# Kernel tuning notes

Measured on AMD Instinct MI355X. Metric: run time of the kernel, lower is better.

The kernel has to match this reference:

```python
import jax, jax.numpy as jnp
import numpy as np

DIM = 512
HEADS = 8
DIM_HEAD = 64
B, N = 4, 2048
EPS = 1e-5


def setup_inputs() -> dict:
    key = jax.random.key(0)
    ks = jax.random.split(key, 6)
    s = 0.02
    x = jax.random.normal(ks[0], (B, N, DIM), dtype=jnp.float32)
    Wq = jax.random.normal(ks[1], (DIM, HEADS * DIM_HEAD), dtype=jnp.float32) * s
    Wkv = jax.random.normal(ks[2], (DIM, 2 * HEADS * DIM_HEAD), dtype=jnp.float32) * s
    Wo = jax.random.normal(ks[3], (HEADS * DIM_HEAD, DIM), dtype=jnp.float32) * s
    bo = jnp.zeros((DIM,), dtype=jnp.float32)
    # gating layer: torch init is weight=0, bias=1; randomize weight slightly for a nontrivial path
    Wg = jax.random.normal(ks[4], (DIM, HEADS * DIM_HEAD), dtype=jnp.float32) * s
    bg = jnp.ones((HEADS * DIM_HEAD,), dtype=jnp.float32)
    gamma = jnp.ones((DIM,), dtype=jnp.float32)
    beta = jnp.zeros((DIM,), dtype=jnp.float32)
    return {"x": x, "Wq": Wq, "Wkv": Wkv, "Wo": Wo, "bo": bo,
            "Wg": Wg, "bg": bg, "gamma": gamma, "beta": beta}


def reference(x, Wq, Wkv, Wo, bo, Wg, bg, gamma, beta):
    h, d = HEADS, DIM_HEAD
    scale = d ** -0.5
    b, n, _ = x.shape

    q = x @ Wq                                   # [b, n, h*d]
    kv = x @ Wkv                                 # [b, n, 2*h*d]
    k, v = jnp.split(kv, 2, axis=-1)

    def split_heads(t):
        return t.reshape(b, n, h, d).transpose(0, 2, 1, 3)  # [b, h, n, d]

    q = split_heads(q) * scale
    k = split_heads(k)
    v = split_heads(v)

    dots = jnp.einsum('bhid,bhjd->bhij', q, k)   # [b, h, n, n]
    attn = jax.nn.softmax(dots, axis=-1)
    out = jnp.einsum('bhij,bhjd->bhid', attn, v)  # [b, h, n, d]
    out = out.transpose(0, 2, 1, 3).reshape(b, n, h * d)

    gates = x @ Wg + bg                           # [b, n, h*d]
    out = out * jax.nn.sigmoid(gates)
    out = out @ Wo + bo                           # [b, n, dim]
    out = x + out

    # LayerNorm over last dim, eps=1e-5 (torch default)
    mu = jnp.mean(out, axis=-1, keepdims=True)
    var = jnp.var(out, axis=-1, keepdims=True)
    out = (out - mu) * jax.lax.rsqrt(var + EPS) * gamma + beta
    return out
```

## Files before the change

kernel.cpp:

```cpp
#include <hip/hip_runtime.h>
#include <hip/hip_bf16.h>
#include <stdint.h>
#include <stddef.h>

#define SEQ   2048
#define NBATCH 4
#define NHEAD  8
#define DMODEL 512

typedef __attribute__((ext_vector_type(8))) short bf16x8;
typedef __attribute__((ext_vector_type(4))) float f32x4;
typedef __attribute__((ext_vector_type(16))) float f32x16;

#define MFMA16(a, b, c) __builtin_amdgcn_mfma_f32_16x16x32_bf16(a, b, c, 0, 0, 0)
#define MFMA32(a, b, c) __builtin_amdgcn_mfma_f32_32x32x16_bf16(a, b, c, 0, 0, 0)

#define QSCALE 0.18033688011112042f

__device__ __forceinline__ float bf2f(ushort u) {
  union { uint32_t i; float f; } v; v.i = ((uint32_t)u) << 16; return v.f;
}
__device__ __forceinline__ ushort f2bf(float f) {
  union { float f; uint32_t i; } v; v.f = f;
  uint32_t u = v.i;
  return (ushort)((u + 0x7fffu + ((u >> 16) & 1u)) >> 16);
}
__device__ __forceinline__ uint32_t cvtpk(float lo, float hi) {
  uint32_t d;
  asm("v_cvt_pk_bf16_f32 %0, %1, %2" : "=v"(d) : "v"(lo), "v"(hi));
  return d;
}

#if __has_builtin(__builtin_amdgcn_global_load_lds)
__device__ __forceinline__ void gload16(const void* g, void* l) {
  __builtin_amdgcn_global_load_lds(
      (const __attribute__((address_space(1))) void*)g,
      (__attribute__((address_space(3))) void*)l, 16, 0, 0);
}
#define GLOAD_DIRECT 1
#else
#define GLOAD_DIRECT 0
#endif

__global__ __launch_bounds__(256) void cvt_k(const float* __restrict__ in,
                                             ushort* __restrict__ out, int n8) {
  int i = blockIdx.x * 256 + threadIdx.x;
  if (i >= n8) return;
  const float4* p = (const float4*)(in + (size_t)i * 8);
  float4 a = p[0], b = p[1];
  union { int4 v; ushort u[8]; } o;
  o.u[0] = f2bf(a.x); o.u[1] = f2bf(a.y); o.u[2] = f2bf(a.z); o.u[3] = f2bf(a.w);
  o.u[4] = f2bf(b.x); o.u[5] = f2bf(b.y); o.u[6] = f2bf(b.z); o.u[7] = f2bf(b.w);
  *(int4*)(out + (size_t)i * 8) = o.v;
}

__global__ __launch_bounds__(256) void wtrans_k(const float* __restrict__ Wq,
                                                const float* __restrict__ Wkv,
                                                const float* __restrict__ Wg,
                                                const float* __restrict__ Wo,
                                                ushort* __restrict__ WT,
                                                ushort* __restrict__ WoT) {
  __shared__ ushort tile[32][33];
  int bx = blockIdx.x;
  const float* W;
  ushort* dst;
  int N, nt;
  if (bx < 16)       { W = Wq;  dst = WT;              N = 512;  nt = bx; }
  else if (bx < 48)  { W = Wkv; dst = WT + 512 * 512;  N = 1024; nt = bx - 16; }
  else if (bx < 64)  { W = Wg;  dst = WT + 1536 * 512; N = 512;  nt = bx - 48; }
  else               { W = Wo;  dst = WoT;             N = 512;  nt = bx - 64; }
  int t = threadIdx.x;
  int n0 = nt * 32, k0 = blockIdx.y * 32;
  int r = t >> 3, c = (t & 7) * 4;
#pragma unroll
  for (int j = 0; j < 4; j++)
    tile[r][c + j] = f2bf(W[(size_t)(k0 + r) * N + n0 + c + j]);
  __syncthreads();
#pragma unroll
  for (int j = 0; j < 4; j++)
    dst[(size_t)(n0 + r) * 512 + k0 + c + j] = tile[c + j][r];
}

__global__ __launch_bounds__(256, 2) void gemm128_k(const ushort* __restrict__ A,
                                                    const ushort* __restrict__ Bt,
                                                    ushort* __restrict__ qb,
                                                    ushort* __restrict__ kb,
                                                    ushort* __restrict__ vT,
                                                    ushort* __restrict__ gsb,
                                                    float* __restrict__ yout,
                                                    const float* __restrict__ bias,
                                                    const float* __restrict__ res,
                                                    int op) {
  __shared__ __align__(16) ushort Sh[4 * 128 * 64];
#define ASB(p) (Sh + (p) * (128 * 64))
#define BSB(p) (Sh + 2 * (128 * 64) + (p) * (128 * 64))
  int t = threadIdx.x;
  int nb = gridDim.x * gridDim.y;
  int bid = blockIdx.y * gridDim.x + blockIdx.x;
  int swz = (bid & 7) * (nb >> 3) + (bid >> 3);
  int row0 = (swz / gridDim.x) * 128, col0 = (swz % gridDim.x) * 128;

  int w = t >> 6, l = t & 63, l31 = l & 31, hi = l >> 5;
  int wm = w >> 1, wn = w & 1;
  f32x16 acc[2][2] = {};

  int srow = t >> 3;
  int ssl = (t & 7) ^ (srow & 7);
  const ushort* Ag = A + (size_t)(row0 + srow) * 512 + ssl * 8;
  const ushort* Bg = Bt + (size_t)(col0 + srow) * 512 + ssl * 8;
  int wslot = __builtin_amdgcn_readfirstlane((t >> 6) << 6);

#if GLOAD_DIRECT
#define STG(p, kt)                                                              \
  do {                                                                          \
    gload16(Ag + (size_t)(kt) * 64 + 0 * 32 * 512, ASB(p) + (wslot +   0) * 8); \
    gload16(Ag + (size_t)(kt) * 64 + 1 * 32 * 512, ASB(p) + (wslot + 256) * 8); \
    gload16(Ag + (size_t)(kt) * 64 + 2 * 32 * 512, ASB(p) + (wslot + 512) * 8); \
    gload16(Ag + (size_t)(kt) * 64 + 3 * 32 * 512, ASB(p) + (wslot + 768) * 8); \
    gload16(Bg + (size_t)(kt) * 64 + 0 * 32 * 512, BSB(p) + (wslot +   0) * 8); \
    gload16(Bg + (size_t)(kt) * 64 + 1 * 32 * 512, BSB(p) + (wslot + 256) * 8); \
    gload16(Bg + (size_t)(kt) * 64 + 2 * 32 * 512, BSB(p) + (wslot + 512) * 8); \
    gload16(Bg + (size_t)(kt) * 64 + 3 * 32 * 512, BSB(p) + (wslot + 768) * 8); \
  } while (0)
#else
#define STG(p, kt)                                                                  \
  do {                                                                              \
    *(int4*)(ASB(p) + (t +   0) * 8) = *(const int4*)(Ag + (size_t)(kt) * 64);      \
    *(int4*)(ASB(p) + (t + 256) * 8) =                                              \
        *(const int4*)(Ag + (size_t)(kt) * 64 + 1 * 32 * 512);                      \
    *(int4*)(ASB(p) + (t + 512) * 8) =                                              \
        *(const int4*)(Ag + (size_t)(kt) * 64 + 2 * 32 * 512);                      \
    *(int4*)(ASB(p) + (t + 768) * 8) =                                              \
        *(const int4*)(Ag + (size_t)(kt) * 64 + 3 * 32 * 512);                      \
    *(int4*)(BSB(p) + (t +   0) * 8) = *(const int4*)(Bg + (size_t)(kt) * 64);      \
    *(int4*)(BSB(p) + (t + 256) * 8) =                                              \
        *(const int4*)(Bg + (size_t)(kt) * 64 + 1 * 32 * 512);                      \
    *(int4*)(BSB(p) + (t + 512) * 8) =                                              \
        *(const int4*)(Bg + (size_t)(kt) * 64 + 2 * 32 * 512);                      \
    *(int4*)(BSB(p) + (t + 768) * 8) =                                              \
        *(const int4*)(Bg + (size_t)(kt) * 64 + 3 * 32 * 512);                      \
  } while (0)
#endif

#define FRAG(Mb, r, s) \
  (*(const bf16x8*)(Mb + ((r) * 64) + ((((s) ^ ((r) & 7))) << 3)))

  STG(0, 0);
  __syncthreads();

  for (int kt = 0; kt < 8; kt++) {
    int p = kt & 1;
    if (kt < 7) STG(p ^ 1, kt + 1);

    bf16x8 bfrag[2][4];
#pragma unroll
    for (int cb = 0; cb < 2; cb++)
#pragma unroll
      for (int kk = 0; kk < 4; kk++)
        bfrag[cb][kk] = FRAG(BSB(p), wn * 64 + cb * 32 + l31, kk * 2 + hi);

    __builtin_amdgcn_s_setprio(1);
#pragma unroll
    for (int rb = 0; rb < 2; rb++) {
      bf16x8 af[4];
#pragma unroll
      for (int kk = 0; kk < 4; kk++)
        af[kk] = FRAG(ASB(p), wm * 64 + rb * 32 + l31, kk * 2 + hi);
#pragma unroll
      for (int kk = 0; kk < 4; kk++) {
        acc[rb][0] = MFMA32(af[kk], bfrag[0][kk], acc[rb][0]);
        acc[rb][1] = MFMA32(af[kk], bfrag[1][kk], acc[rb][1]);
      }
    }
    __builtin_amdgcn_s_setprio(0);

    if (kt < 7) __syncthreads();
  }
#undef STG
#undef FRAG

  if (op == 10 && col0 >= 1024 && col0 < 1536) {
    __syncthreads();
    ushort* lt = Sh;
#pragma unroll
    for (int rb = 0; rb < 2; rb++)
#pragma unroll
      for (int cb = 0; cb < 2; cb++)
#pragma unroll
        for (int e = 0; e < 16; e++) {
          int rr = (e & 3) + 8 * (e >> 2) + 4 * hi;
          int rowL = wm * 64 + rb * 32 + rr;
          int colL = wn * 64 + cb * 32 + l31;
          lt[colL * 136 + rowL] = f2bf(acc[rb][cb][e]);
        }
    __syncthreads();
    int b_ = row0 >> 11;
    int nb0 = row0 & 2047;
#pragma unroll
    for (int r = 0; r < 8; r++) {
      int lin = r * 256 + t;
      int dcol = lin >> 4, n8 = lin & 15;
      int vcol = (col0 - 1024) + dcol;
      int hh = vcol >> 6, dd = vcol & 63;
      bf16x8 v = *(const bf16x8*)(lt + dcol * 136 + n8 * 8);
      *(bf16x8*)(vT + (((size_t)(b_ * 8 + hh) * 64) + dd) * 2048 + nb0 + n8 * 8) = v;
    }
  } else {
#pragma unroll
    for (int rb = 0; rb < 2; rb++) {
#pragma unroll
      for (int cb = 0; cb < 2; cb++) {
#pragma unroll
        for (int e = 0; e < 16; e++) {
          int rr = (e & 3) + 8 * (e >> 2) + 4 * hi;
          int row = row0 + wm * 64 + rb * 32 + rr;
          int col = col0 + wn * 64 + cb * 32 + l31;
          float v = acc[rb][cb][e];
          if (op == 3) {
            v += bias[col] + res[(size_t)row * 512 + col];
            yout[(size_t)row * 512 + col] = v;
          } else {
            if (col0 < 512) {
              qb[(size_t)row * 512 + col] = f2bf(v * QSCALE);
            } else if (col0 < 1024) {
              kb[(size_t)row * 512 + (col - 512)] = f2bf(v);
            } else {
              v += bias[col - 1536];
              v = 1.f / (1.f + __expf(-v));
              gsb[(size_t)row * 512 + (col - 1536)] = f2bf(v);
            }
          }
        }
      }
    }
  }
#undef ASB
#undef BSB
}

__global__ __launch_bounds__(512) void attn_k(const ushort* __restrict__ q,
                                              const ushort* __restrict__ kbuf,
                                              const ushort* __restrict__ vT,
                                              const ushort* __restrict__ gs,
                                              ushort* __restrict__ gated) {
  __shared__ __align__(16) ushort Kl[2][64][72];
  __shared__ __align__(16) ushort Vl[2][64][72];
  int t = threadIdx.x;
  int bid = blockIdx.x;
  int swz = (bid & 7) * 32 + (bid >> 3);
  int qt = swz & 7, bh = swz >> 3;
  int b = bh >> 3, h = bh & 7;
  int q0 = qt * 256;
  int w = t >> 6, l = t & 63;
  int l31 = l & 31, hi = l >> 5;
  size_t base_n = (size_t)b * SEQ;

  const ushort* qp = q + (base_n + q0 + w * 32 + l31) * 512 + h * 64 + hi * 8;
  bf16x8 qf[4];
#pragma unroll
  for (int kd = 0; kd < 4; kd++)
    qf[kd] = *(const bf16x8*)(qp + kd * 16);

  bf16x8 vones;
#pragma unroll
  for (int j = 0; j < 8; j++) vones[j] = (short)0x3F80;

  f32x16 acco0 = {}, acco1 = {}, acco2 = {};

  int srow = t >> 3, c8 = (t & 7) * 8;
  const ushort* kg = kbuf + (base_n + srow) * 512 + h * 64 + c8;
  const ushort* vg = vT + ((size_t)bh * 64 + srow) * 2048 + c8;

  int4 kA = *(const int4*)(kg);
  int4 vA = *(const int4*)(vg);
  *(int4*)((char*)Kl[0] + srow * 144 + c8 * 2) = kA;
  *(int4*)((char*)Vl[0] + srow * 144 + c8 * 2) = vA;
  kA = *(const int4*)(kg + (size_t)64 * 512);
  vA = *(const int4*)(vg + 64);
  __syncthreads();

  int p = 0;
  for (int jt = 0; jt < SEQ / 64; jt++) {
    f32x16 s0 = {}, s1 = {};
    __builtin_amdgcn_s_setprio(1);
#pragma unroll
    for (int kd = 0; kd < 4; kd++) {
      bf16x8 k0 = *(const bf16x8*)((const char*)Kl[p] + l31 * 144 + kd * 32 + hi * 16);
      bf16x8 k1 = *(const bf16x8*)((const char*)Kl[p] + (32 + l31) * 144 + kd * 32 + hi * 16);
      s0 = MFMA32(k0, qf[kd], s0);
      s1 = MFMA32(k1, qf[kd], s1);
    }
    __builtin_amdgcn_s_setprio(0);

    if (jt < SEQ / 64 - 1) {
      *(int4*)((char*)Kl[p ^ 1] + srow * 144 + c8 * 2) = kA;
      *(int4*)((char*)Vl[p ^ 1] + srow * 144 + c8 * 2) = vA;
    }

    uint32_t pk[16];
#pragma unroll
    for (int sg = 0; sg < 4; sg++) {
#pragma unroll
      for (int u = 0; u < 2; u++) {
        float a = __builtin_amdgcn_exp2f(s0[(sg << 2) | (u << 1)]);
        float c = __builtin_amdgcn_exp2f(s0[(sg << 2) | (u << 1) | 1]);
        pk[sg * 2 + u] = cvtpk(a, c);
      }
    }
#pragma unroll
    for (int sg = 0; sg < 4; sg++) {
#pragma unroll
      for (int u = 0; u < 2; u++) {
        float a = __builtin_amdgcn_exp2f(s1[(sg << 2) | (u << 1)]);
        float c = __builtin_amdgcn_exp2f(s1[(sg << 2) | (u << 1) | 1]);
        pk[8 + sg * 2 + u] = cvtpk(a, c);
      }
    }

    __builtin_amdgcn_s_setprio(1);
#pragma unroll
    for (int jk = 0; jk < 4; jk++) {
      uint32_t x0 = pk[(2 * jk) * 2 + 0], y0 = pk[(2 * jk + 1) * 2 + 0];
      uint32_t x1 = pk[(2 * jk) * 2 + 1], y1 = pk[(2 * jk + 1) * 2 + 1];
      asm("v_permlane32_swap_b32 %0, %1" : "+v"(x0), "+v"(y0));
      asm("v_permlane32_swap_b32 %0, %1" : "+v"(x1), "+v"(y1));
      union { bf16x8 v; uint32_t u[4]; } pa;
      pa.u[0] = x0; pa.u[1] = x1; pa.u[2] = y0; pa.u[3] = y1;
      bf16x8 v0 = *(const bf16x8*)((const char*)Vl[p] + l31 * 144 + jk * 32 + hi * 16);
      bf16x8 v1 = *(const bf16x8*)((const char*)Vl[p] + (32 + l31) * 144 + jk * 32 + hi * 16);
      acco0 = MFMA32(pa.v, v0, acco0);
      acco1 = MFMA32(pa.v, v1, acco1);
      acco2 = MFMA32(pa.v, vones, acco2);
    }
    __builtin_amdgcn_s_setprio(0);

    if (jt < SEQ / 64 - 1) {
      __syncthreads();
      if (jt < SEQ / 64 - 2) {
        kA = *(const int4*)(kg + (size_t)(jt + 2) * 64 * 512);
        vA = *(const int4*)(vg + (jt + 2) * 64);
      }
      p ^= 1;
    }
  }

#pragma unroll
  for (int e = 0; e < 16; e++) {
    int qr = (e & 3) + 8 * (e >> 2) + 4 * hi;
    size_t row = base_n + q0 + w * 32 + qr;
    int col = h * 64 + l31;
    float rcp = 1.f / acco2[e];
    float v0 = acco0[e] * rcp * bf2f(gs[row * 512 + col]);
    float v1 = acco1[e] * rcp * bf2f(gs[row * 512 + col + 32]);
    gated[row * 512 + col] = f2bf(v0);
    gated[row * 512 + col + 32] = f2bf(v1);
  }
}

__global__ __launch_bounds__(256) void ln_k(const float* __restrict__ y,
                                            const float* __restrict__ gamma,
                                            const float* __restrict__ beta,
                                            float* __restrict__ out) {
  int w = threadIdx.x >> 6, l = threadIdx.x & 63;
  size_t row = (size_t)blockIdx.x * 4 + w;
  const float4* yp = (const float4*)(y + row * 512);
  float4 a = yp[l * 2], b = yp[l * 2 + 1];
  float f[8] = {a.x, a.y, a.z, a.w, b.x, b.y, b.z, b.w};
  float sm = 0.f, sq = 0.f;
#pragma unroll
  for (int j = 0; j < 8; j++) { sm += f[j]; sq += f[j] * f[j]; }
#pragma unroll
  for (int off = 1; off < 64; off <<= 1) {
    sm += __shfl_xor(sm, off);
    sq += __shfl_xor(sq, off);
  }
  float mean = sm * (1.f / 512.f);
  float var = sq * (1.f / 512.f) - mean * mean;
  float rs = rsqrtf(var + 1e-5f);
  float4 g0 = ((const float4*)gamma)[l * 2], g1 = ((const float4*)gamma)[l * 2 + 1];
  float4 b0 = ((const float4*)beta)[l * 2],  b1 = ((const float4*)beta)[l * 2 + 1];
  float4 o0, o1;
  o0.x = (f[0] - mean) * rs * g0.x + b0.x;
  o0.y = (f[1] - mean) * rs * g0.y + b0.y;
  o0.z = (f[2] - mean) * rs * g0.z + b0.z;
  o0.w = (f[3] - mean) * rs * g0.w + b0.w;
  o1.x = (f[4] - mean) * rs * g1.x + b1.x;
  o1.y = (f[5] - mean) * rs * g1.y + b1.y;
  o1.z = (f[6] - mean) * rs * g1.z + b1.z;
  o1.w = (f[7] - mean) * rs * g1.w + b1.w;
  float4* op = (float4*)(out + row * 512);
  op[l * 2] = o0;
  op[l * 2 + 1] = o1;
}

extern "C" void kernel_launch(void* const* d_in, const int* in_sizes, int n_in,
                              void* d_out, int out_size, void* d_ws, size_t ws_size,
                              hipStream_t stream) {
  (void)in_sizes; (void)n_in; (void)out_size; (void)ws_size;
  const float* x     = (const float*)d_in[0];
  const float* Wq    = (const float*)d_in[1];
  const float* Wkv   = (const float*)d_in[2];
  const float* Wo    = (const float*)d_in[3];
  const float* bo    = (const float*)d_in[4];
  const float* Wg    = (const float*)d_in[5];
  const float* bg    = (const float*)d_in[6];
  const float* gamma = (const float*)d_in[7];
  const float* beta  = (const float*)d_in[8];

  char* ws = (char*)d_ws;
  ushort* xb    = (ushort*)(ws);
  ushort* qbuf  = (ushort*)(ws + (8u  << 20));
  ushort* kbuf  = (ushort*)(ws + (16u << 20));
  ushort* vT    = (ushort*)(ws + (32u << 20));
  ushort* gsb   = (ushort*)(ws + (40u << 20));
  ushort* gated = (ushort*)(ws + (48u << 20));
  float*  y     = (float*)(ws + (56u << 20));
  ushort* WT    = (ushort*)(ws + (72u << 20));
  ushort* WoT   = (ushort*)(ws + (74u << 20));

  cvt_k<<<(NBATCH * SEQ * DMODEL / 8 + 255) / 256, 256, 0, stream>>>(
      x, xb, NBATCH * SEQ * DMODEL / 8);

  wtrans_k<<<dim3(80, 16), 256, 0, stream>>>(Wq, Wkv, Wg, Wo, WT, WoT);

  gemm128_k<<<dim3(16, 64), 256, 0, stream>>>(xb, WT, qbuf, kbuf, vT, gsb,
                                              nullptr, bg, nullptr, 10);

  attn_k<<<256, 512, 0, stream>>>(qbuf, kbuf, vT, gsb, gated);

  gemm128_k<<<dim3(4, 64), 256, 0, stream>>>(gated, WoT, nullptr, nullptr,
                                             nullptr, nullptr, y, bo, x, 3);

  ln_k<<<(NBATCH * SEQ) / 4, 256, 0, stream>>>(y, gamma, beta, (float*)d_out);
}
```

Before: 132.2 us.

## Software-pipeline attention loop: overlap next QK^T with current softmax and PV

Restructures the attention inner loop into a two-stage software pipeline with triple-buffered K/V tiles in LDS. The QK^T MFMAs for the next tile are issued before the exp/pack and PV MFMAs of the current tile, so matrix-core work can overlap the transcendental work. It also removes the setprio hints and raises LDS use to three buffers, with extra score registers held live, which may cut occupancy or add register pressure.

```diff
diff --git a/kernel.cpp b/kernel.cpp
--- a/kernel.cpp
+++ b/kernel.cpp
@@ -243,8 +243,8 @@
                                               const ushort* __restrict__ vT,
                                               const ushort* __restrict__ gs,
                                               ushort* __restrict__ gated) {
-  __shared__ __align__(16) ushort Kl[2][64][72];
-  __shared__ __align__(16) ushort Vl[2][64][72];
+  __shared__ __align__(16) ushort Kl[3][64][72];
+  __shared__ __align__(16) ushort Vl[3][64][72];
   int t = threadIdx.x;
   int bid = blockIdx.x;
   int swz = (bid & 7) * 32 + (bid >> 3);
@@ -271,6 +271,75 @@
   const ushort* kg = kbuf + (base_n + srow) * 512 + h * 64 + c8;
   const ushort* vg = vT + ((size_t)bh * 64 + srow) * 2048 + c8;
 
+#define QK_PHASE(KB, S0, S1)                                                   \
+  do {                                                                         \
+    _Pragma("unroll")                                                          \
+    for (int kd = 0; kd < 4; kd++) {                                           \
+      bf16x8 k0 = *(const bf16x8*)((KB) + l31 * 144 + kd * 32 + hi * 16);      \
+      bf16x8 k1 = *(const bf16x8*)((KB) + (32 + l31) * 144 + kd * 32 + hi * 16);\
+      S0 = MFMA32(k0, qf[kd], S0);                                             \
+      S1 = MFMA32(k1, qf[kd], S1);                                             \
+    }                                                                          \
+  } while (0)
+
+#define SM_PHASE(S0, S1, PK)                                                   \
+  do {                                                                         \
+    _Pragma("unroll")                                                          \
+    for (int sg = 0; sg < 4; sg++) {                                           \
+      _Pragma("unroll")                                                        \
+      for (int u = 0; u < 2; u++) {                                            \
+        float a = __builtin_amdgcn_exp2f(S0[(sg << 2) | (u << 1)]);            \
+        float c = __builtin_amdgcn_exp2f(S0[(sg << 2) | (u << 1) | 1]);        \
+        PK[sg * 2 + u] = cvtpk(a, c);                                          \
+      }                                                                        \
+    }                                                                          \
+    _Pragma("unroll")                                                          \
+    for (int sg = 0; sg < 4; sg++) {                                           \
+      _Pragma("unroll")                                                        \
+      for (int u = 0; u < 2; u++) {                                            \
+        float a = __builtin_amdgcn_exp2f(S1[(sg << 2) | (u << 1)]);            \
+        float c = __builtin_amdgcn_exp2f(S1[(sg << 2) | (u << 1) | 1]);        \
+        PK[8 + sg * 2 + u] = cvtpk(a, c);                                      \
+      }                                                                        \
+    }                                                                          \
+  } while (0)
+
+#define PV_PHASE(VB, PK)                                                       \
+  do {                                                                         \
+    _Pragma("unroll")                                                          \
+    for (int jk = 0; jk < 4; jk++) {                                           \
+      uint32_t x0 = PK[(2 * jk) * 2 + 0], y0 = PK[(2 * jk + 1) * 2 + 0];       \
+      uint32_t x1 = PK[(2 * jk) * 2 + 1], y1 = PK[(2 * jk + 1) * 2 + 1];       \
+      asm("v_permlane32_swap_b32 %0, %1" : "+v"(x0), "+v"(y0));                \
+      asm("v_permlane32_swap_b32 %0, %1" : "+v"(x1), "+v"(y1));                \
+      union { bf16x8 v; uint32_t u[4]; } pa;                                   \
+      pa.u[0] = x0; pa.u[1] = x1; pa.u[2] = y0; pa.u[3] = y1;                  \
+      bf16x8 v0 = *(const bf16x8*)((VB) + l31 * 144 + jk * 32 + hi * 16);      \
+      bf16x8 v1 = *(const bf16x8*)((VB) + (32 + l31) * 144 + jk * 32 + hi * 16);\
+      acco0 = MFMA32(pa.v, v0, acco0);                                         \
+      acco1 = MFMA32(pa.v, v1, acco1);                                         \
+      acco2 = MFMA32(pa.v, vones, acco2);                                      \
+    }                                                                          \
+  } while (0)
+
+#define STAGE_LDS()                                                            \
+  do {                                                                         \
+    *(int4*)(kT + srow * 144 + c8 * 2) = kA;                                   \
+    *(int4*)(vT_ + srow * 144 + c8 * 2) = vA;                                  \
+  } while (0)
+
+#define LOADT(n)                                                               \
+  do {                                                                         \
+    kA = *(const int4*)(kg + (size_t)(n) * 64 * 512);                          \
+    vA = *(const int4*)(vg + (n) * 64);                                        \
+  } while (0)
+
+#define ROTATE()                                                               \
+  do {                                                                         \
+    char* tk = kC; kC = kN; kN = kT; kT = tk;                                  \
+    char* tv = vC; vC = vN; vN = vT_; vT_ = tv;                                \
+  } while (0)
+
   int4 kA = *(const int4*)(kg);
   int4 vA = *(const int4*)(vg);
   *(int4*)((char*)Kl[0] + srow * 144 + c8 * 2) = kA;
@@ -279,70 +348,48 @@
   vA = *(const int4*)(vg + 64);
   __syncthreads();
 
-  int p = 0;
-  for (int jt = 0; jt < SEQ / 64; jt++) {
-    f32x16 s0 = {}, s1 = {};
-    __builtin_amdgcn_s_setprio(1);
-#pragma unroll
-    for (int kd = 0; kd < 4; kd++) {
-      bf16x8 k0 = *(const bf16x8*)((const char*)Kl[p] + l31 * 144 + kd * 32 + hi * 16);
-      bf16x8 k1 = *(const bf16x8*)((const char*)Kl[p] + (32 + l31) * 144 + kd * 32 + hi * 16);
-      s0 = MFMA32(k0, qf[kd], s0);
-      s1 = MFMA32(k1, qf[kd], s1);
+  f32x16 sA0 = {}, sA1 = {}, sB0, sB1;
+  QK_PHASE((const char*)Kl[0], sA0, sA1);
+  *(int4*)((char*)Kl[1] + srow * 144 + c8 * 2) = kA;
+  *(int4*)((char*)Vl[1] + srow * 144 + c8 * 2) = vA;
+  kA = *(const int4*)(kg + (size_t)128 * 512);
+  vA = *(const int4*)(vg + 128);
+  __syncthreads();
+
+  char* kC = (char*)Kl[0]; char* kN = (char*)Kl[1]; char* kT = (char*)Kl[2];
+  char* vC = (char*)Vl[0]; char* vN = (char*)Vl[1]; char* vT_ = (char*)Vl[2];
+
+  for (int jt2 = 0; jt2 < 16; jt2++) {
+    int jt = jt2 * 2;
+    {
+      sB0 = (f32x16){}; sB1 = (f32x16){};
+      QK_PHASE(kN, sB0, sB1);
+      uint32_t pk[16];
+      SM_PHASE(sA0, sA1, pk);
+      if (jt + 2 < 32) STAGE_LDS();
+      PV_PHASE(vC, pk);
+      if (jt + 3 < 32) LOADT(jt + 3);
+      ROTATE();
+      __syncthreads();
     }
-    __builtin_amdgcn_s_setprio(0);
-
-    if (jt < SEQ / 64 - 1) {
-      *(int4*)((char*)Kl[p ^ 1] + srow * 144 + c8 * 2) = kA;
-      *(int4*)((char*)Vl[p ^ 1] + srow * 144 + c8 * 2) = vA;
-    }
-
-    uint32_t pk[16];
-#pragma unroll
-    for (int sg = 0; sg < 4; sg++) {
-#pragma unroll
-      for (int u = 0; u < 2; u++) {
-        float a = __builtin_amdgcn_exp2f(s0[(sg << 2) | (u << 1)]);
-        float c = __builtin_amdgcn_exp2f(s0[(sg << 2) | (u << 1) | 1]);
-        pk[sg * 2 + u] = cvtpk(a, c);
-      }
-    }
-#pragma unroll
-    for (int sg = 0; sg < 4; sg++) {
-#pragma unroll
-      for (int u = 0; u < 2; u++) {
-        float a = __builtin_amdgcn_exp2f(s1[(sg << 2) | (u << 1)]);
-        float c = __builtin_amdgcn_exp2f(s1[(sg << 2) | (u << 1) | 1]);
-        pk[8 + sg * 2 + u] = cvtpk(a, c);
-      }
-    }
-
-    __builtin_amdgcn_s_setprio(1);
-#pragma unroll
-    for (int jk = 0; jk < 4; jk++) {
-      uint32_t x0 = pk[(2 * jk) * 2 + 0], y0 = pk[(2 * jk + 1) * 2 + 0];
-      uint32_t x1 = pk[(2 * jk) * 2 + 1], y1 = pk[(2 * jk + 1) * 2 + 1];
-      asm("v_permlane32_swap_b32 %0, %1" : "+v"(x0), "+v"(y0));
-      asm("v_permlane32_swap_b32 %0, %1" : "+v"(x1), "+v"(y1));
-      union { bf16x8 v; uint32_t u[4]; } pa;
-      pa.u[0] = x0; pa.u[1] = x1; pa.u[2] = y0; pa.u[3] = y1;
-      bf16x8 v0 = *(const bf16x8*)((const char*)Vl[p] + l31 * 144 + jk * 32 + hi * 16);
-      bf16x8 v1 = *(const bf16x8*)((const char*)Vl[p] + (32 + l31) * 144 + jk * 32 + hi * 16);
-      acco0 = MFMA32(pa.v, v0, acco0);
-      acco1 = MFMA32(pa.v, v1, acco1);
-      acco2 = MFMA32(pa.v, vones, acco2);
-    }
-    __builtin_amdgcn_s_setprio(0);
-
-    if (jt < SEQ / 64 - 1) {
-      __syncthreads();
-      if (jt < SEQ / 64 - 2) {
-        kA = *(const int4*)(kg + (size_t)(jt + 2) * 64 * 512);
-        vA = *(const int4*)(vg + (jt + 2) * 64);
-      }
-      p ^= 1;
+    {
+      sA0 = (f32x16){}; sA1 = (f32x16){};
+      if (jt + 2 < 32) QK_PHASE(kN, sA0, sA1);
+      uint32_t pk[16];
+      SM_PHASE(sB0, sB1, pk);
+      if (jt + 3 < 32) STAGE_LDS();
+      PV_PHASE(vC, pk);
+      if (jt + 4 < 32) LOADT(jt + 4);
+      ROTATE();
+      if (jt2 < 15) __syncthreads();
     }
   }
+#undef QK_PHASE
+#undef SM_PHASE
+#undef PV_PHASE
+#undef STAGE_LDS
+#undef LOADT
+#undef ROTATE
 
 #pragma unroll
   for (int e = 0; e < 16; e++) {
```

Result: no change. 133.0 us (+0.6%).
